# Kernel tuning notes

Hardware: AMD Instinct MI355X
Metric: run time of the kernel (lower is better)

Reference implementation:

```python
import jax, jax.numpy as jnp
import numpy as np

NEG_SLOPE = 0.2  # PyG GATConv default leaky_relu slope


def gat_layer(x, src, dst, W, a_src, a_dst, n_nodes, heads, ch):
    # x: [N, in_dim]; W: [in_dim, heads*ch]
    h = (x @ W).reshape(n_nodes, heads, ch)              # [N, H, C]
    e_s = jnp.einsum('nhc,hc->nh', h, a_src)             # [N, H]
    e_d = jnp.einsum('nhc,hc->nh', h, a_dst)             # [N, H]
    e = jax.nn.leaky_relu(e_s[src] + e_d[dst], NEG_SLOPE)  # [E, H]
    # segment softmax over incoming edges of each destination node
    m = jax.lax.stop_gradient(jax.ops.segment_max(e, dst, num_segments=n_nodes))
    w = jnp.exp(e - m[dst])                              # [E, H]
    z = jax.ops.segment_sum(w, dst, num_segments=n_nodes)  # [N, H]
    alpha = w / z[dst]                                   # [E, H]
    msg = h[src] * alpha[:, :, None]                     # [E, H, C]
    out = jax.ops.segment_sum(msg, dst, num_segments=n_nodes)  # [N, H, C]
    return out


def setup_inputs() -> dict:
    key = jax.random.key(0)
    ks = jax.random.split(key, 12)
    N, E, D, H = 50000, 800000, 128, 4
    x = jax.random.normal(ks[0], (N, D), dtype=jnp.float32)
    edge_index = jax.random.randint(ks[1], (2, E), 0, N, dtype=jnp.int64)
    s1 = 1.0 / np.sqrt(D)
    s2 = 1.0 / np.sqrt(D * H)
    W1 = jax.random.normal(ks[2], (D, H * D), dtype=jnp.float32) * s1
    a1_src = jax.random.normal(ks[3], (H, D), dtype=jnp.float32) * s1
    a1_dst = jax.random.normal(ks[4], (H, D), dtype=jnp.float32) * s1
    b1 = jax.random.normal(ks[5], (H * D,), dtype=jnp.float32) * 0.01
    W2 = jax.random.normal(ks[6], (H * D, D), dtype=jnp.float32) * s2
    a2_src = jax.random.normal(ks[7], (1, D), dtype=jnp.float32) * s1
    a2_dst = jax.random.normal(ks[8], (1, D), dtype=jnp.float32) * s1
    b2 = jax.random.normal(ks[9], (D,), dtype=jnp.float32) * 0.01
    fc_w = jax.random.normal(ks[10], (D, 1), dtype=jnp.float32) * s1
    fc_b = jax.random.normal(ks[11], (1,), dtype=jnp.float32) * 0.01
    return {"x": x, "edge_index": edge_index, "W1": W1, "a1_src": a1_src,
            "a1_dst": a1_dst, "b1": b1, "W2": W2, "a2_src": a2_src,
            "a2_dst": a2_dst, "b2": b2, "fc_w": fc_w, "fc_b": fc_b}


def reference(x, edge_index, W1, a1_src, a1_dst, b1, W2, a2_src, a2_dst, b2, fc_w, fc_b):
    N, D = x.shape
    H = a1_src.shape[0]
    # add self-loops (PyG GATConv default add_self_loops=True)
    loop = jnp.arange(N, dtype=edge_index.dtype)
    src = jnp.concatenate([edge_index[0], loop])
    dst = jnp.concatenate([edge_index[1], loop])
    # conv1: heads=4, concat=True -> [N, H*D]
    h1 = gat_layer(x, src, dst, W1, a1_src, a1_dst, N, H, D)
    h1 = jax.nn.relu(h1.reshape(N, H * D) + b1)
    # dropout p=0.2 is identity in eval mode
    # conv2: heads=1 -> [N, D]
    h2 = gat_layer(h1, src, dst, W2, a2_src, a2_dst, N, 1, D)
    h2 = h2.reshape(N, D) + b2
    return h2 @ fc_w + fc_b  # [N, 1]
```

## Files before the change

kernel.cpp:

```cpp
#include <hip/hip_runtime.h>
#include <cstdint>
#include <cstddef>

constexpr int kN   = 50000;
constexpr int kE   = 800000;
constexpr int kEt  = kE + kN;
constexpr float kSlope = 0.2f;
constexpr int kScanB = (kN + 255) / 256;
constexpr int kConvB = (kN * 16 + 255) / 256;
constexpr int kHistB = (kEt + 255) / 256;
constexpr int kQuarB = (kN * 16 + 255) / 256;
constexpr int kHBlk  = 256;
constexpr int kChunk = (kEt + kHBlk - 1) / kHBlk;
constexpr int kHalfN = kN / 2;

typedef __attribute__((ext_vector_type(8))) short bf8_t;
typedef __attribute__((ext_vector_type(4))) float f4_t;
typedef __attribute__((ext_vector_type(2))) float f2_t;

__device__ __align__(16) unsigned short g_xb[(size_t)kN * 128];
__device__ __align__(16) unsigned short g_aggx[(size_t)kN * 512];
__device__ __align__(16) unsigned short g_w1t[4 * 128 * 128];
__device__ __align__(16) float g_u[3][512];
__device__ __align__(16) float g_es1[kN * 4];
__device__ __align__(16) float g_ed1[kN * 4];
__device__ __align__(16) float2 g_sp[kN];
__device__ float g_ed2[kN];
__device__ float g_c0;
__device__ __align__(16) float g_p1s[4 * 128];
__device__ __align__(16) float g_p1d[4 * 128];
__device__ int g_deg[kN];
__device__ int g_ptr[kN + 1];
__device__ int g_rank[kEt];
__device__ __align__(16) unsigned g_bhist[(size_t)kHBlk * kHalfN];
__device__ __align__(16) unsigned g_bbase[(size_t)kHBlk * kHalfN];
__device__ int g_srcs[kEt];
__device__ int g_bsum[kScanB];

__device__ __forceinline__ float lrelu(float x) { return x > 0.f ? x : kSlope * x; }

__device__ __forceinline__ bf8_t bf8_zero() {
  uint4 z = make_uint4(0u, 0u, 0u, 0u);
  return *(bf8_t*)&z;
}

__device__ __forceinline__ unsigned short f2bf1(float v) {
  unsigned u = __float_as_uint(v);
  unsigned r = (u + 0x7FFFu + ((u >> 16) & 1u)) >> 16;
  return (unsigned short)r;
}

__global__ __launch_bounds__(256) void k_hist(const int* __restrict__ ei) {
  __shared__ unsigned sh[kHalfN];
  const int b = blockIdx.x, t = threadIdx.x;
  for (int i = t; i < kHalfN; i += 256) sh[i] = 0u;
  __syncthreads();
  const int beg = b * kChunk, end = min(beg + kChunk, kEt);
  for (int e = beg + t; e < end; e += 256) {
    int d = (e < kE) ? ei[kE + e] : e - kE;
    unsigned inc = (d & 1) ? 0x10000u : 1u;
    unsigned old = atomicAdd(&sh[d >> 1], inc);
    g_rank[e] = (d & 1) ? (int)(old >> 16) : (int)(old & 0xFFFFu);
  }
  __syncthreads();
  unsigned* dst = g_bhist + (size_t)b * kHalfN;
  for (int i = t; i < kHalfN; i += 256) dst[i] = sh[i];
}

__global__ __launch_bounds__(256) void k_pass2() {
  const int i = blockIdx.x * 256 + threadIdx.x;
  if (i >= kHalfN) return;
  unsigned c0 = 0, c1 = 0;
#pragma unroll 4
  for (int b = 0; b < kHBlk; ++b) {
    unsigned v = g_bhist[(size_t)b * kHalfN + i];
    g_bbase[(size_t)b * kHalfN + i] = c0 | (c1 << 16);
    c0 += v & 0xFFFFu;
    c1 += v >> 16;
  }
  *(int2*)&g_deg[2 * i] = make_int2((int)c0, (int)c1);
}

__global__ __launch_bounds__(256) void k_init(const float* __restrict__ x,
    const float* __restrict__ W1, const float* __restrict__ W2,
    const float* __restrict__ a1s, const float* __restrict__ a1d,
    const float* __restrict__ a2s, const float* __restrict__ a2d,
    const float* __restrict__ b2, const float* __restrict__ fcw,
    const float* __restrict__ fcb) {
  const int b = blockIdx.x, t = threadIdx.x;
  if (b < 197) {
    int i = b * 256 + t;
    if (i < kN) {
      g_sp[i] = make_float2(0.f, 0.f);
      g_ed2[i] = 0.f;
    }
  } else if (b < 453) {
    int gid = (b - 197) * 256 + t;
    int h = gid >> 14, rem = gid & 16383;
    int c = rem >> 7, j = rem & 127;
    float v = W1[(size_t)c * 512 + h * 128 + j];
    g_w1t[((size_t)h * 128 + j) * 128 + c] = f2bf1(v);
  } else if (b < 457) {
    int gid = (b - 453) * 256 + t;
    int which = gid >> 9, idx = gid & 511;
    int h = idx >> 7, k = idx & 127;
    const float* a = which ? a1d : a1s;
    const float* wrow = W1 + (size_t)k * 512 + h * 128;
    float s = 0.f;
#pragma unroll 8
    for (int c = 0; c < 128; ++c) s += wrow[c] * a[h * 128 + c];
    (which ? g_p1d : g_p1s)[idx] = s;
  } else if (b < 463) {
    int gid = (b - 457) * 256 + t;
    if (gid < 1536) {
      int v = gid >> 9, k = gid & 511;
      const float* vv = v == 0 ? a2s : v == 1 ? a2d : fcw;
      const float* wrow = W2 + (size_t)k * 128;
      float s = 0.f;
#pragma unroll 8
      for (int c = 0; c < 128; ++c) s += wrow[c] * vv[c];
      g_u[v][k] = s;
    }
  } else if (b < 464) {
    if (t < 64) {
      float s = b2[t] * fcw[t] + b2[64 + t] * fcw[64 + t];
#pragma unroll
      for (int off = 32; off > 0; off >>= 1) s += __shfl_down(s, off);
      if (t == 0) g_c0 = s + fcb[0];
    }
  } else {
    int g = (b - 464) * 256 + t;
    if (g < kN * 16) {
      const float* xp = x + (size_t)g * 8;
      float4 f0 = *(const float4*)xp;
      float4 f1 = *(const float4*)(xp + 4);
      unsigned w0 = (unsigned)f2bf1(f0.x) | ((unsigned)f2bf1(f0.y) << 16);
      unsigned w1 = (unsigned)f2bf1(f0.z) | ((unsigned)f2bf1(f0.w) << 16);
      unsigned w2 = (unsigned)f2bf1(f1.x) | ((unsigned)f2bf1(f1.y) << 16);
      unsigned w3 = (unsigned)f2bf1(f1.z) | ((unsigned)f2bf1(f1.w) << 16);
      *(uint4*)(g_xb + (size_t)g * 8) = make_uint4(w0, w1, w2, w3);
    }
  }
}

__device__ __forceinline__ void scores1_body(const float* __restrict__ x,
                                             int bid, int t) {
  const int lane = t & 63;
  const int qt = lane >> 4, ql = lane & 15;
  const int n = ((bid * 256 + t) >> 6) * 4 + qt;
  if (n >= kN) return;
  const float* xp = x + (size_t)n * 128 + ql * 8;
  float4 xa = *(const float4*)xp;
  float4 xb = *(const float4*)(xp + 4);
  float s[4], d[4];
#pragma unroll
  for (int h = 0; h < 4; ++h) {
    const float* ps = g_p1s + h * 128 + ql * 8;
    const float* pd = g_p1d + h * 128 + ql * 8;
    s[h] = xa.x * ps[0] + xa.y * ps[1] + xa.z * ps[2] + xa.w * ps[3]
         + xb.x * ps[4] + xb.y * ps[5] + xb.z * ps[6] + xb.w * ps[7];
    d[h] = xa.x * pd[0] + xa.y * pd[1] + xa.z * pd[2] + xa.w * pd[3]
         + xb.x * pd[4] + xb.y * pd[5] + xb.z * pd[6] + xb.w * pd[7];
  }
#pragma unroll
  for (int off = 1; off < 16; off <<= 1) {
#pragma unroll
    for (int h = 0; h < 4; ++h) {
      s[h] += __shfl_xor(s[h], off);
      d[h] += __shfl_xor(d[h], off);
    }
  }
  if (ql == 0) {
    *(float4*)(g_es1 + (size_t)n * 4) = make_float4(s[0], s[1], s[2], s[3]);
    *(float4*)(g_ed1 + (size_t)n * 4) = make_float4(d[0], d[1], d[2], d[3]);
  }
}

__global__ __launch_bounds__(256) void k_scanA(const float* __restrict__ x) {
  __shared__ int s[256];
  const int b = blockIdx.x, t = threadIdx.x;
  if (b >= kScanB) {
    scores1_body(x, b - kScanB, t);
    return;
  }
  const int i = b * 256 + t;
  int d = (i < kN) ? g_deg[i] : 0;
  s[t] = d;
  __syncthreads();
  for (int off = 1; off < 256; off <<= 1) {
    int v = s[t];
    int u = (t >= off) ? s[t - off] : 0;
    __syncthreads();
    s[t] = v + u;
    __syncthreads();
  }
  if (t == 255) g_bsum[b] = s[255];
  if (i < kN) g_ptr[i] = s[t] - d;
}

__global__ __launch_bounds__(256) void k_scanC() {
  __shared__ int s[256];
  const int b = blockIdx.x, t = threadIdx.x;
  int v = (t < kScanB) ? g_bsum[t] : 0;
  s[t] = v;
  __syncthreads();
  for (int off = 1; off < 256; off <<= 1) {
    int a = s[t];
    int u = (t >= off) ? s[t - off] : 0;
    __syncthreads();
    s[t] = a + u;
    __syncthreads();
  }
  const int boff = (b > 0) ? s[b - 1] : 0;
  __syncthreads();
  const int i = b * 256 + t;
  if (i < kN) g_ptr[i] = g_ptr[i] + boff;
  if (b == 0 && t == 0) g_ptr[kN] = kEt;
}

__global__ __launch_bounds__(256) void k_scatter(const int* __restrict__ ei) {
  int e = blockIdx.x * 256 + threadIdx.x;
  if (e >= kEt) return;
  int s, d;
  if (e < kE) { s = ei[e]; d = ei[kE + e]; } else { s = d = e - kE; }
  const int b = e / kChunk;
  unsigned base = g_bbase[(size_t)b * kHalfN + (d >> 1)];
  base = (d & 1) ? (base >> 16) : (base & 0xFFFFu);
  g_srcs[g_ptr[d] + (int)base + g_rank[e]] = s;
}

__global__ __launch_bounds__(256) void k_agg1x() {
  const int lane = threadIdx.x & 63;
  const int qt = lane >> 4, ql = lane & 15;
  const int n = ((blockIdx.x * 256 + threadIdx.x) >> 6) * 4 + qt;
  if (n >= kN) return;
  const int beg = g_ptr[n], end = g_ptr[n + 1];
  const float4 ed = *(const float4*)(g_ed1 + (size_t)n * 4);
  const int lbase = qt * 16;
  float z0 = 0.f, z1 = 0.f, z2 = 0.f, z3 = 0.f;
  f2_t acc[4][4] = {};
  for (int base = beg; base < end; base += 16) {
    const int cnt = min(16, end - base);
    int s = 0;
    float w0 = 0.f, w1 = 0.f, w2 = 0.f, w3 = 0.f;
    if (ql < cnt) {
      s = g_srcs[base + ql];
      float4 es = *(const float4*)(g_es1 + (size_t)s * 4);
      w0 = __expf(lrelu(es.x + ed.x));
      w1 = __expf(lrelu(es.y + ed.y));
      w2 = __expf(lrelu(es.z + ed.z));
      w3 = __expf(lrelu(es.w + ed.w));
      z0 += w0; z1 += w1; z2 += w2; z3 += w3;
    }
    auto proc = [&](const uint4& uu, int e) {
      float b0 = __shfl(w0, lbase + e), b1 = __shfl(w1, lbase + e);
      float b2 = __shfl(w2, lbase + e), b3 = __shfl(w3, lbase + e);
      f2_t bb0 = b0, bb1 = b1, bb2 = b2, bb3 = b3;
      unsigned ws[4] = {uu.x, uu.y, uu.z, uu.w};
#pragma unroll
      for (int d = 0; d < 4; ++d) {
        f2_t fv;
        fv[0] = __uint_as_float(ws[d] << 16);
        fv[1] = __uint_as_float(ws[d] & 0xFFFF0000u);
        acc[0][d] += bb0 * fv;
        acc[1][d] += bb1 * fv;
        acc[2][d] += bb2 * fv;
        acc[3][d] += bb3 * fv;
      }
    };
    int e = 0;
    for (; e + 4 <= cnt; e += 4) {
      int sj0 = __shfl(s, lbase + e);
      int sj1 = __shfl(s, lbase + e + 1);
      int sj2 = __shfl(s, lbase + e + 2);
      int sj3 = __shfl(s, lbase + e + 3);
      uint4 u0 = *(const uint4*)(g_xb + (size_t)sj0 * 128 + ql * 8);
      uint4 u1 = *(const uint4*)(g_xb + (size_t)sj1 * 128 + ql * 8);
      uint4 u2 = *(const uint4*)(g_xb + (size_t)sj2 * 128 + ql * 8);
      uint4 u3 = *(const uint4*)(g_xb + (size_t)sj3 * 128 + ql * 8);
      proc(u0, e);
      proc(u1, e + 1);
      proc(u2, e + 2);
      proc(u3, e + 3);
    }
    for (; e < cnt; ++e) {
      int sj = __shfl(s, lbase + e);
      uint4 uu = *(const uint4*)(g_xb + (size_t)sj * 128 + ql * 8);
      proc(uu, e);
    }
  }
#pragma unroll
  for (int off = 1; off < 16; off <<= 1) {
    z0 += __shfl_xor(z0, off); z1 += __shfl_xor(z1, off);
    z2 += __shfl_xor(z2, off); z3 += __shfl_xor(z3, off);
  }
  const float iz[4] = {1.f / z0, 1.f / z1, 1.f / z2, 1.f / z3};
  const size_t nb = (size_t)n * 512 + ql * 8;
#pragma unroll
  for (int h = 0; h < 4; ++h) {
    unsigned wd[4];
#pragma unroll
    for (int d = 0; d < 4; ++d) {
      f2_t v = acc[h][d] * iz[h];
      wd[d] = (unsigned)f2bf1(v[0]) | ((unsigned)f2bf1(v[1]) << 16);
    }
    *(uint4*)(g_aggx + nb + h * 128) = make_uint4(wd[0], wd[1], wd[2], wd[3]);
  }
}

__global__ __launch_bounds__(256) void k_fused(const float* __restrict__ b1) {
  __shared__ float sred[2][64][3];
  const int t = threadIdx.x;
  const int lane = t & 63, w = t >> 6;
  const int wrow = w >> 1, wcol = w & 1;
  const int ln15 = lane & 15, q = lane >> 4, qo = q * 8;
  const int row0 = blockIdx.y * 64;
  const int h = blockIdx.z;

  float part[2][4][3] = {};
  f4_t h1acc[2][4] = {};
#pragma unroll
  for (int ks = 0; ks < 128; ks += 32) {
    bf8_t ah[2];
#pragma unroll
    for (int i = 0; i < 2; ++i) {
      int r = row0 + wrow * 32 + i * 16 + ln15;
      ah[i] = bf8_zero();
      if (r < kN)
        ah[i] = *(const bf8_t*)&g_aggx[(size_t)r * 512 + h * 128 + ks + qo];
    }
#pragma unroll
    for (int j = 0; j < 4; ++j) {
      size_t gb = ((size_t)h * 128 + wcol * 64 + j * 16 + ln15) * 128 + ks + qo;
      bf8_t bh = *(const bf8_t*)&g_w1t[gb];
#pragma unroll
      for (int i = 0; i < 2; ++i)
        h1acc[i][j] = __builtin_amdgcn_mfma_f32_16x16x32_bf16(ah[i], bh, h1acc[i][j], 0, 0, 0);
    }
  }
#pragma unroll
  for (int j = 0; j < 4; ++j) {
    int col = h * 128 + wcol * 64 + j * 16 + ln15;
    float bv = b1[col];
    float u0 = g_u[0][col], u1 = g_u[1][col], u2 = g_u[2][col];
#pragma unroll
    for (int i = 0; i < 2; ++i)
#pragma unroll
      for (int reg = 0; reg < 4; ++reg) {
        float v = fmaxf(h1acc[i][j][reg] + bv, 0.f);
        part[i][reg][0] += v * u0;
        part[i][reg][1] += v * u1;
        part[i][reg][2] += v * u2;
      }
  }
#pragma unroll
  for (int off = 1; off < 16; off <<= 1)
#pragma unroll
    for (int i = 0; i < 2; ++i)
#pragma unroll
      for (int reg = 0; reg < 4; ++reg)
#pragma unroll
        for (int v = 0; v < 3; ++v)
          part[i][reg][v] += __shfl_xor(part[i][reg][v], off);
  if (ln15 == 0) {
#pragma unroll
    for (int i = 0; i < 2; ++i)
#pragma unroll
      for (int reg = 0; reg < 4; ++reg) {
        int rl = wrow * 32 + i * 16 + q * 4 + reg;
#pragma unroll
        for (int v = 0; v < 3; ++v) sred[wcol][rl][v] = part[i][reg][v];
      }
  }
  __syncthreads();
  if (t < 192) {
    int row = t / 3, v = t - row * 3;
    float s = sred[0][row][v] + sred[1][row][v];
    int r = row0 + row;
    if (r < kN) {
      float* dst = v == 0 ? &g_sp[r].x : v == 1 ? &g_ed2[r] : &g_sp[r].y;
      atomicAdd(dst, s);
    }
  }
}

__global__ __launch_bounds__(256) void k_agg2s(float* __restrict__ out) {
  const int lane = threadIdx.x & 63;
  const int qt = lane >> 4, ql = lane & 15;
  const int n = ((blockIdx.x * 256 + threadIdx.x) >> 6) * 4 + qt;
  if (n >= kN) return;
  const int beg = g_ptr[n], end = g_ptr[n + 1];
  const float ed = g_ed2[n];
  float zp = 0.f, num = 0.f;
  for (int slot = beg + ql; slot < end; slot += 16) {
    int s = g_srcs[slot];
    float2 sp = g_sp[s];
    float w = __expf(lrelu(sp.x + ed));
    zp += w;
    num += w * sp.y;
  }
#pragma unroll
  for (int off = 1; off < 16; off <<= 1) {
    zp  += __shfl_xor(zp, off);
    num += __shfl_xor(num, off);
  }
  if (ql == 0) out[n] = num / zp + g_c0;
}

extern "C" void kernel_launch(void* const* d_in, const int* in_sizes, int n_in,
                              void* d_out, int out_size, void* d_ws, size_t ws_size,
                              hipStream_t stream) {
  const float* x   = (const float*)d_in[0];
  const int*   ei  = (const int*)d_in[1];
  const float* W1  = (const float*)d_in[2];
  const float* a1s = (const float*)d_in[3];
  const float* a1d = (const float*)d_in[4];
  const float* b1  = (const float*)d_in[5];
  const float* W2  = (const float*)d_in[6];
  const float* a2s = (const float*)d_in[7];
  const float* a2d = (const float*)d_in[8];
  const float* b2  = (const float*)d_in[9];
  const float* fcw = (const float*)d_in[10];
  const float* fcb = (const float*)d_in[11];
  float* out = (float*)d_out;
  (void)d_ws; (void)ws_size; (void)in_sizes; (void)n_in; (void)out_size;

  k_hist<<<kHBlk, 256, 0, stream>>>(ei);
  k_init<<<464 + kConvB, 256, 0, stream>>>(x, W1, W2, a1s, a1d,
                                           a2s, a2d, b2, fcw, fcb);
  k_pass2<<<(kHalfN + 255) / 256, 256, 0, stream>>>();
  k_scanA<<<kScanB + kQuarB, 256, 0, stream>>>(x);
  k_scanC<<<kScanB, 256, 0, stream>>>();
  k_scatter<<<kHistB, 256, 0, stream>>>(ei);

  k_agg1x<<<kQuarB, 256, 0, stream>>>();

  dim3 gf(1, (kN + 63) / 64, 4);
  k_fused<<<gf, 256, 0, stream>>>(b1);

  k_agg2s<<<kQuarB, 256, 0, stream>>>(out);
}
```

Baseline: 274.8 us.

## Partition degree histogram by destination range to shrink shared-memory footprint

The per-block histogram now covers only a quarter of the node range, so each block keeps a 25K-entry shared array instead of 100KB. There are fewer edge chunks (64 instead of 256), and each chunk is scanned by 4 blocks that filter edges to their own range. The smaller shared array allows more blocks per CU and cuts the per-chunk histogram write-out and the pass2 prefix-scan length. The cost is that every block reads four times as many edges as it keeps.

```diff
diff --git a/kernel.cpp b/kernel.cpp
--- a/kernel.cpp
+++ b/kernel.cpp
@@ -10,9 +10,12 @@
 constexpr int kConvB = (kN * 16 + 255) / 256;
 constexpr int kHistB = (kEt + 255) / 256;
 constexpr int kQuarB = (kN * 16 + 255) / 256;
-constexpr int kHBlk  = 256;
-constexpr int kChunk = (kEt + kHBlk - 1) / kHBlk;
-constexpr int kHalfN = kN / 2;
+constexpr int kHChunks = 64;
+constexpr int kChunk   = (kEt + kHChunks - 1) / kHChunks;
+constexpr int kHRanges = 4;
+constexpr int kRangeN  = kN / kHRanges;
+constexpr int kRangeH  = kRangeN / 2;
+constexpr int kHalfN   = kN / 2;
 
 typedef __attribute__((ext_vector_type(8))) short bf8_t;
 typedef __attribute__((ext_vector_type(4))) float f4_t;
@@ -32,8 +35,8 @@
 __device__ int g_deg[kN];
 __device__ int g_ptr[kN + 1];
 __device__ int g_rank[kEt];
-__device__ __align__(16) unsigned g_bhist[(size_t)kHBlk * kHalfN];
-__device__ __align__(16) unsigned g_bbase[(size_t)kHBlk * kHalfN];
+__device__ __align__(16) unsigned g_bhist[(size_t)kHChunks * kHalfN];
+__device__ __align__(16) unsigned g_bbase[(size_t)kHChunks * kHalfN];
 __device__ int g_srcs[kEt];
 __device__ int g_bsum[kScanB];
 
@@ -51,20 +54,25 @@
 }
 
 __global__ __launch_bounds__(256) void k_hist(const int* __restrict__ ei) {
-  __shared__ unsigned sh[kHalfN];
+  __shared__ unsigned sh[kRangeH];
   const int b = blockIdx.x, t = threadIdx.x;
-  for (int i = t; i < kHalfN; i += 256) sh[i] = 0u;
-  __syncthreads();
-  const int beg = b * kChunk, end = min(beg + kChunk, kEt);
+  const int chunk = b & (kHChunks - 1);
+  const int rr = b >> 6;
+  const int lo = rr * kRangeN, hi = lo + kRangeN;
+  for (int i = t; i < kRangeH; i += 256) sh[i] = 0u;
+  __syncthreads();
+  const int beg = chunk * kChunk, end = min(beg + kChunk, kEt);
   for (int e = beg + t; e < end; e += 256) {
     int d = (e < kE) ? ei[kE + e] : e - kE;
-    unsigned inc = (d & 1) ? 0x10000u : 1u;
-    unsigned old = atomicAdd(&sh[d >> 1], inc);
-    g_rank[e] = (d & 1) ? (int)(old >> 16) : (int)(old & 0xFFFFu);
-  }
-  __syncthreads();
-  unsigned* dst = g_bhist + (size_t)b * kHalfN;
-  for (int i = t; i < kHalfN; i += 256) dst[i] = sh[i];
+    if (d >= lo && d < hi) {
+      unsigned inc = (d & 1) ? 0x10000u : 1u;
+      unsigned old = atomicAdd(&sh[(d - lo) >> 1], inc);
+      g_rank[e] = (d & 1) ? (int)(old >> 16) : (int)(old & 0xFFFFu);
+    }
+  }
+  __syncthreads();
+  unsigned* dst = g_bhist + (size_t)chunk * kHalfN + rr * kRangeH;
+  for (int i = t; i < kRangeH; i += 256) dst[i] = sh[i];
 }
 
 __global__ __launch_bounds__(256) void k_pass2() {
@@ -72,7 +80,7 @@
   if (i >= kHalfN) return;
   unsigned c0 = 0, c1 = 0;
 #pragma unroll 4
-  for (int b = 0; b < kHBlk; ++b) {
+  for (int b = 0; b < kHChunks; ++b) {
     unsigned v = g_bhist[(size_t)b * kHalfN + i];
     g_bbase[(size_t)b * kHalfN + i] = c0 | (c1 << 16);
     c0 += v & 0xFFFFu;
@@ -425,7 +433,7 @@
   float* out = (float*)d_out;
   (void)d_ws; (void)ws_size; (void)in_sizes; (void)n_in; (void)out_size;
 
-  k_hist<<<kHBlk, 256, 0, stream>>>(ei);
+  k_hist<<<kHChunks * kHRanges, 256, 0, stream>>>(ei);
   k_init<<<464 + kConvB, 256, 0, stream>>>(x, W1, W2, a1s, a1d,
                                            a2s, a2d, b2, fcw, fcb);
   k_pass2<<<(kHalfN + 255) / 256, 256, 0, stream>>>();
```

After: 260.6 us (median of 2 runs). 1.05x faster.
